# Performance work log

Hardware: AMD Instinct MI355X
Metric: run time of the kernel (lower is better)

## Reference

```python
import jax, jax.numpy as jnp
import numpy as np

BN_EPS = 1e-5

def _tok2img(f):
    # f: [197, 768] tokens (CLS first). Drop CLS, transpose, reshape -> [1, 768, 14, 14].
    # fv4[0, c, i, j] = f[1 + i*14 + j, c], identical to the original triple loop.
    return f[1:].T.reshape(1, 768, 14, 14)

def _resize(x, s):
    # PyTorch F.interpolate(mode='bilinear', align_corners=False) == jax.image.resize 'bilinear'
    n, c, h, w = x.shape
    return jax.image.resize(x, (n, c, h * s, w * s), method='bilinear')

def _conv_relu_bn(x, conv_w, conv_b, g, b, m, v):
    y = jax.lax.conv_general_dilated(x, conv_w, window_strides=(1, 1), padding='SAME',
                                     dimension_numbers=('NCHW', 'OIHW', 'NCHW'))
    y = y + conv_b[None, :, None, None]
    y = jax.nn.relu(y)
    # BatchNorm2d(1) in eval mode with running stats
    scale = g * jax.lax.rsqrt(v + BN_EPS)
    return y * scale[None, :, None, None] + (b - m * scale)[None, :, None, None]

def setup_inputs() -> dict:
    key = jax.random.key(0)
    ks = jax.random.split(key, 4)
    return {
        'x': jax.random.normal(ks[0], (14, 14), dtype=jnp.float32),
        'fv': jax.random.normal(ks[1], (4, 197, 768), dtype=jnp.float32),
        'conv_w': jax.random.normal(ks[2], (1, 769, 3, 3), dtype=jnp.float32) * 0.02,
        'conv_b': jnp.zeros((1,), jnp.float32),
        'bn_gamma': jnp.ones((1,), jnp.float32),
        'bn_beta': jnp.zeros((1,), jnp.float32),
        'bn_mean': jnp.zeros((1,), jnp.float32),
        'bn_var': jnp.ones((1,), jnp.float32),
        'W_w': jax.random.normal(ks[3], (224, 224), dtype=jnp.float32) * 0.05,
        'W_b': jnp.zeros((224,), jnp.float32),
    }

def reference(x, fv, conv_w, conv_b, bn_gamma, bn_beta, bn_mean, bn_var, W_w, W_b):
    h = x[None, None]  # [1,1,14,14]
    # skip features, pre-resized to match current resolution at each stage
    feats = (
        _tok2img(fv[3]),              # 14x14
        _resize(_tok2img(fv[2]), 2),  # 28x28
        _resize(_tok2img(fv[1]), 4),  # 56x56
        _resize(_tok2img(fv[0]), 8),  # 112x112
    )
    for f in feats:
        h = jnp.concatenate([h, f], axis=1)  # [1,769,H,W]
        h = _conv_relu_bn(h, conv_w, conv_b, bn_gamma, bn_beta, bn_mean, bn_var)
        h = _resize(h, 2)
    # Linear(224,224) over the last dim of [1,1,224,224]
    h = jnp.einsum('nchw,ow->ncho', h, W_w) + W_b
    return jax.nn.sigmoid(h)
```

## Files before the change

### kernel.cpp

```cpp
#include <hip/hip_runtime.h>
#include <math.h>


#define BN_EPS 1e-5f

__device__ __forceinline__ float clampf(float x, float lo, float hi) {
    return fminf(fmaxf(x, lo), hi);
}

__device__ __forceinline__ float sampleB(const float* __restrict__ Bt, float fy, float fx) {
    int y0 = (int)fy; float by = fy - (float)y0; int y1 = min(y0 + 1, 13);
    int x0 = (int)fx; float bx = fx - (float)x0; int x1 = min(x0 + 1, 13);
    return (1.f - by) * ((1.f - bx) * Bt[y0 * 14 + x0] + bx * Bt[y0 * 14 + x1])
         + by         * ((1.f - bx) * Bt[y1 * 14 + x0] + bx * Bt[y1 * 14 + x1]);
}

__device__ __forceinline__ float stage_pixel(int i, int j, int H,
                                             const float* __restrict__ hsrc, int srcH, int doUp,
                                             const float* __restrict__ sB,
                                             const float* __restrict__ cw, float bias) {
    float featScale = 14.0f / (float)H;
    float srcMax = (float)(srcH - 1);
    float acc = bias;

#pragma unroll
    for (int a = 0; a < 3; ++a) {
        int p = i + a - 1;
        if (p < 0 || p >= H) continue;
        float fy = clampf(((float)p + 0.5f) * featScale - 0.5f, 0.f, 13.f);
        int hy0 = 0, hy1 = 0; float fhy = 0.f;
        if (doUp) {
            float hy = clampf(((float)p + 0.5f) * 0.5f - 0.5f, 0.f, srcMax);
            hy0 = (int)hy; fhy = hy - (float)hy0; hy1 = min(hy0 + 1, srcH - 1);
        }
#pragma unroll
        for (int bq = 0; bq < 3; ++bq) {
            int q = j + bq - 1;
            if (q < 0 || q >= H) continue;
            int t = a * 3 + bq;

            float fx = clampf(((float)q + 0.5f) * featScale - 0.5f, 0.f, 13.f);
            float bv = sampleB(sB + t * 196, fy, fx);

            float hval;
            if (doUp) {
                float hx = clampf(((float)q + 0.5f) * 0.5f - 0.5f, 0.f, srcMax);
                int hx0 = (int)hx; float fhx = hx - (float)hx0; int hx1 = min(hx0 + 1, srcH - 1);
                hval = (1.f - fhy) * ((1.f - fhx) * hsrc[hy0 * srcH + hx0] + fhx * hsrc[hy0 * srcH + hx1])
                     + fhy         * ((1.f - fhx) * hsrc[hy1 * srcH + hx0] + fhx * hsrc[hy1 * srcH + hx1]);
            } else {
                hval = hsrc[p * srcH + q];
            }
            acc += cw[t] * hval + bv;
        }
    }
    return acc;
}

__device__ __forceinline__ void srcRange(int dlo, int dhi, int srcH, int& slo, int& shi) {
    int H = 2 * srcH;
    int p0 = max(dlo - 1, 0), p1 = min(dhi + 1, H - 1);
    float h0 = fmaxf(((float)p0 + 0.5f) * 0.5f - 0.5f, 0.f);
    float h1 = fmaxf(((float)p1 + 0.5f) * 0.5f - 0.5f, 0.f);
    slo = (int)h0;
    shi = min((int)h1 + 1, srcH - 1);
}

__global__ __launch_bounds__(256)
void compute_B_kernel(const float* __restrict__ fv, const float* __restrict__ conv_w,
                      const float* __restrict__ W_w,
                      float* __restrict__ gB, float* __restrict__ gWT) {
    int blk = blockIdx.x;
    int s = blk / 196;
    int uv = blk % 196;
    const float* fvrow = fv + ((size_t)(3 - s) * 197 + 1 + uv) * 768;
    int tid = threadIdx.x;

    if (tid < 64) {
        int idx = blk * 64 + tid;
        int o = idx / 224, w = idx % 224;
        gWT[w * 224 + o] = W_w[idx];
    }

    float part[9];
#pragma unroll
    for (int t = 0; t < 9; ++t) part[t] = 0.f;
    for (int k = tid; k < 768; k += 256) {
        float fval = fvrow[k];
        const float* w = conv_w + (size_t)(1 + k) * 9;
#pragma unroll
        for (int t = 0; t < 9; ++t) part[t] += fval * w[t];
    }
#pragma unroll
    for (int t = 0; t < 9; ++t) {
#pragma unroll
        for (int off = 32; off > 0; off >>= 1)
            part[t] += __shfl_down(part[t], off, 64);
    }
    __shared__ float red[4][9];
    int wave = tid >> 6, lane = tid & 63;
    if (lane == 0) {
#pragma unroll
        for (int t = 0; t < 9; ++t) red[wave][t] = part[t];
    }
    __syncthreads();
    if (tid < 9)
        gB[s * 1764 + tid * 196 + uv] = red[0][tid] + red[1][tid] + red[2][tid] + red[3][tid];
}

__global__ __launch_bounds__(1024, 1)
void refine_kernel(const float* __restrict__ x,
                   const float* __restrict__ conv_w, const float* __restrict__ conv_b,
                   const float* __restrict__ bng, const float* __restrict__ bnb,
                   const float* __restrict__ bnm, const float* __restrict__ bnv,
                   const float* __restrict__ W_b,
                   const float* __restrict__ gB, const float* __restrict__ gWT,
                   float* __restrict__ out) {
    __shared__ float sB[4 * 9 * 196];
    __shared__ float y1s[196];
    __shared__ float y2s[784];
    __shared__ float y3s[3136];
    __shared__ float y4loc[3 * 112];
    __shared__ float hrow[2][224];
    __shared__ float partial[4][224];

    int tid = threadIdx.x;
    int b = blockIdx.x;

    int y4lo = max(b - 1, 0), y4hi = min(b + 1, 111);
    int r3lo, r3hi; srcRange(y4lo, y4hi, 56, r3lo, r3hi);
    int r2lo, r2hi; srcRange(r3lo, r3hi, 28, r2lo, r2hi);
    int r1lo, r1hi; srcRange(r2lo, r2hi, 14, r1lo, r1hi);

    for (int k = tid; k < 7056; k += 1024) sB[k] = gB[k];

    float cw[9];
#pragma unroll
    for (int t = 0; t < 9; ++t) cw[t] = conv_w[t];
    float bias = conv_b[0];
    float scale = bng[0] * rsqrtf(bnv[0] + BN_EPS);
    float shift = bnb[0] - bnm[0] * scale;
    __syncthreads();

    {
        int n = (r1hi - r1lo + 1) * 14;
        if (tid < n) {
            int i = r1lo + tid / 14, j = tid % 14;
            float acc = stage_pixel(i, j, 14, x, 14, 0, sB, cw, bias);
            y1s[i * 14 + j] = fmaxf(acc, 0.f) * scale + shift;
        }
    }
    __syncthreads();

    {
        int n = (r2hi - r2lo + 1) * 28;
        if (tid < n) {
            int i = r2lo + tid / 28, j = tid % 28;
            float acc = stage_pixel(i, j, 28, y1s, 14, 1, sB + 1764, cw, bias);
            y2s[i * 28 + j] = fmaxf(acc, 0.f) * scale + shift;
        }
    }
    __syncthreads();

    {
        int n = (r3hi - r3lo + 1) * 56;
        if (tid < n) {
            int i = r3lo + tid / 56, j = tid % 56;
            float acc = stage_pixel(i, j, 56, y2s, 28, 1, sB + 2 * 1764, cw, bias);
            y3s[i * 56 + j] = fmaxf(acc, 0.f) * scale + shift;
        }
    }
    __syncthreads();

    {
        int n = (y4hi - y4lo + 1) * 112;
        if (tid < n) {
            int i = y4lo + tid / 112, j = tid % 112;
            float acc = stage_pixel(i, j, 112, y3s, 56, 1, sB + 3 * 1764, cw, bias);
            y4loc[(i - (b - 1)) * 112 + j] = fmaxf(acc, 0.f) * scale + shift;
        }
    }
    __syncthreads();

    if (tid < 2 * 224) {
        int rr = tid / 224, w = tid % 224;
        int r = 2 * b + rr;
        float hy = clampf(((float)r + 0.5f) * 0.5f - 0.5f, 0.f, 111.f);
        int yy0 = (int)hy; float fy = hy - (float)yy0; int yy1 = min(yy0 + 1, 111);
        float hx = clampf(((float)w + 0.5f) * 0.5f - 0.5f, 0.f, 111.f);
        int xx0 = (int)hx; float fx = hx - (float)xx0; int xx1 = min(xx0 + 1, 111);
        int s0 = yy0 - (b - 1), s1 = yy1 - (b - 1);
        hrow[rr][w] = (1.f - fy) * ((1.f - fx) * y4loc[s0 * 112 + xx0] + fx * y4loc[s0 * 112 + xx1])
                    + fy         * ((1.f - fx) * y4loc[s1 * 112 + xx0] + fx * y4loc[s1 * 112 + xx1]);
    }
    __syncthreads();

    if (tid < 896) {
        int q = tid / 224, o = tid % 224;
        int rr = q >> 1, half = q & 1;
        float acc = half ? 0.f : W_b[o];
        const float* hr = hrow[rr];
        int w0 = half * 112;
        for (int w = w0; w < w0 + 112; ++w)
            acc += hr[w] * gWT[w * 224 + o];
        partial[q][o] = acc;
    }
    __syncthreads();

    if (tid < 448) {
        int rr = tid / 224, o = tid % 224;
        float v = partial[rr * 2][o] + partial[rr * 2 + 1][o];
        out[(size_t)(2 * b + rr) * 224 + o] = 1.f / (1.f + expf(-v));
    }
}

extern "C" void kernel_launch(void* const* d_in, const int* in_sizes, int n_in,
                              void* d_out, int out_size, void* d_ws, size_t ws_size,
                              hipStream_t stream) {
    (void)in_sizes; (void)n_in; (void)out_size; (void)ws_size;
    const float* x      = (const float*)d_in[0];
    const float* fv     = (const float*)d_in[1];
    const float* conv_w = (const float*)d_in[2];
    const float* conv_b = (const float*)d_in[3];
    const float* bng    = (const float*)d_in[4];
    const float* bnb    = (const float*)d_in[5];
    const float* bnm    = (const float*)d_in[6];
    const float* bnv    = (const float*)d_in[7];
    const float* W_w    = (const float*)d_in[8];
    const float* W_b    = (const float*)d_in[9];
    float* out = (float*)d_out;

    float* ws  = (float*)d_ws;
    float* gB  = ws;
    float* gWT = ws + 7056;

    compute_B_kernel<<<784, 256, 0, stream>>>(fv, conv_w, W_w, gB, gWT);
    refine_kernel<<<112, 1024, 0, stream>>>(x, conv_w, conv_b, bng, bnb, bnm, bnv,
                                            W_b, gB, gWT, out);
}
```

Before: 90.15 us.

## Fold horizontal upsample into linear weights and load only needed B rows

Precomputes a 112x224 weight matrix that merges the final horizontal bilinear upsample with the Linear layer. The GEMV now runs on the three 112-wide y4 rows, and the vertical interpolation is applied afterwards on the partial results. Each block also copies only the B-table rows its stage ranges need instead of the full 7056-entry table, and stage 1 uses a direct non-interpolated path. The aim is fewer global loads per block and roughly half the GEMV work, at the cost of computing a third y4 row's dot product and extra partial-buffer shared memory.

Measured after the change: 85.89 us. -4.7%, faster.

```diff
diff --git a/kernel.cpp b/kernel.cpp
--- a/kernel.cpp
+++ b/kernel.cpp
@@ -16,7 +16,7 @@
 }
 
 __device__ __forceinline__ float stage_pixel(int i, int j, int H,
-                                             const float* __restrict__ hsrc, int srcH, int doUp,
+                                             const float* __restrict__ hsrc, int srcH,
                                              const float* __restrict__ sB,
                                              const float* __restrict__ cw, float bias) {
     float featScale = 14.0f / (float)H;
@@ -28,11 +28,8 @@
         int p = i + a - 1;
         if (p < 0 || p >= H) continue;
         float fy = clampf(((float)p + 0.5f) * featScale - 0.5f, 0.f, 13.f);
-        int hy0 = 0, hy1 = 0; float fhy = 0.f;
-        if (doUp) {
-            float hy = clampf(((float)p + 0.5f) * 0.5f - 0.5f, 0.f, srcMax);
-            hy0 = (int)hy; fhy = hy - (float)hy0; hy1 = min(hy0 + 1, srcH - 1);
-        }
+        float hy = clampf(((float)p + 0.5f) * 0.5f - 0.5f, 0.f, srcMax);
+        int hy0 = (int)hy; float fhy = hy - (float)hy0; int hy1 = min(hy0 + 1, srcH - 1);
 #pragma unroll
         for (int bq = 0; bq < 3; ++bq) {
             int q = j + bq - 1;
@@ -42,15 +39,10 @@
             float fx = clampf(((float)q + 0.5f) * featScale - 0.5f, 0.f, 13.f);
             float bv = sampleB(sB + t * 196, fy, fx);
 
-            float hval;
-            if (doUp) {
-                float hx = clampf(((float)q + 0.5f) * 0.5f - 0.5f, 0.f, srcMax);
-                int hx0 = (int)hx; float fhx = hx - (float)hx0; int hx1 = min(hx0 + 1, srcH - 1);
-                hval = (1.f - fhy) * ((1.f - fhx) * hsrc[hy0 * srcH + hx0] + fhx * hsrc[hy0 * srcH + hx1])
-                     + fhy         * ((1.f - fhx) * hsrc[hy1 * srcH + hx0] + fhx * hsrc[hy1 * srcH + hx1]);
-            } else {
-                hval = hsrc[p * srcH + q];
-            }
+            float hx = clampf(((float)q + 0.5f) * 0.5f - 0.5f, 0.f, srcMax);
+            int hx0 = (int)hx; float fhx = hx - (float)hx0; int hx1 = min(hx0 + 1, srcH - 1);
+            float hval = (1.f - fhy) * ((1.f - fhx) * hsrc[hy0 * srcH + hx0] + fhx * hsrc[hy0 * srcH + hx1])
+                       + fhy         * ((1.f - fhx) * hsrc[hy1 * srcH + hx0] + fhx * hsrc[hy1 * srcH + hx1]);
             acc += cw[t] * hval + bv;
         }
     }
@@ -66,20 +58,39 @@
     shi = min((int)h1 + 1, srcH - 1);
 }
 
+__device__ __forceinline__ void bRange(int dlo, int dhi, int H, int& lo, int& hi) {
+    float sc = 14.f / (float)H;
+    int p0 = max(dlo - 1, 0), p1 = min(dhi + 1, H - 1);
+    float f0 = clampf(((float)p0 + 0.5f) * sc - 0.5f, 0.f, 13.f);
+    float f1 = clampf(((float)p1 + 0.5f) * sc - 0.5f, 0.f, 13.f);
+    lo = (int)f0;
+    hi = min((int)f1 + 1, 13);
+}
+
 __global__ __launch_bounds__(256)
 void compute_B_kernel(const float* __restrict__ fv, const float* __restrict__ conv_w,
                       const float* __restrict__ W_w,
-                      float* __restrict__ gB, float* __restrict__ gWT) {
+                      float* __restrict__ gB, float* __restrict__ gWTf) {
     int blk = blockIdx.x;
     int s = blk / 196;
     int uv = blk % 196;
     const float* fvrow = fv + ((size_t)(3 - s) * 197 + 1 + uv) * 768;
     int tid = threadIdx.x;
 
-    if (tid < 64) {
-        int idx = blk * 64 + tid;
-        int o = idx / 224, w = idx % 224;
-        gWT[w * 224 + o] = W_w[idx];
+    if (tid < 32) {
+        int idx = blk * 32 + tid;
+        int o = idx % 224, xx = idx / 224;
+        float acc = 0.f;
+#pragma unroll
+        for (int d = -1; d <= 2; ++d) {
+            int w = 2 * xx + d;
+            if (w < 0 || w > 223) continue;
+            float hx = clampf(((float)w + 0.5f) * 0.5f - 0.5f, 0.f, 111.f);
+            int xx0 = (int)hx; float fx = hx - (float)xx0; int xx1 = min(xx0 + 1, 111);
+            float c = (xx0 == xx ? 1.f - fx : 0.f) + (xx1 == xx ? fx : 0.f);
+            acc += c * W_w[o * 224 + w];
+        }
+        gWTf[xx * 224 + o] = acc;
     }
 
     float part[9];
@@ -114,15 +125,14 @@
                    const float* __restrict__ bng, const float* __restrict__ bnb,
                    const float* __restrict__ bnm, const float* __restrict__ bnv,
                    const float* __restrict__ W_b,
-                   const float* __restrict__ gB, const float* __restrict__ gWT,
+                   const float* __restrict__ gB, const float* __restrict__ gWTf,
                    float* __restrict__ out) {
     __shared__ float sB[4 * 9 * 196];
     __shared__ float y1s[196];
     __shared__ float y2s[784];
     __shared__ float y3s[3136];
     __shared__ float y4loc[3 * 112];
-    __shared__ float hrow[2][224];
-    __shared__ float partial[4][224];
+    __shared__ float partial[12 * 224];
 
     int tid = threadIdx.x;
     int b = blockIdx.x;
@@ -132,7 +142,25 @@
     int r2lo, r2hi; srcRange(r3lo, r3hi, 28, r2lo, r2hi);
     int r1lo, r1hi; srcRange(r2lo, r2hi, 14, r1lo, r1hi);
 
-    for (int k = tid; k < 7056; k += 1024) sB[k] = gB[k];
+    int bl0 = max(r1lo - 1, 0), bh0 = min(r1hi + 1, 13);
+    int bl1, bh1; bRange(r2lo, r2hi, 28, bl1, bh1);
+    int bl2, bh2; bRange(r3lo, r3hi, 56, bl2, bh2);
+    int bl3, bh3; bRange(y4lo, y4hi, 112, bl3, bh3);
+
+    {
+        int bl[4] = {bl0, bl1, bl2, bl3}, bh[4] = {bh0, bh1, bh2, bh3};
+#pragma unroll
+        for (int s4 = 0; s4 < 4; ++s4) {
+            int nrw = (bh[s4] - bl[s4] + 1) * 14;
+            int n = 9 * nrw;
+            int base = s4 * 1764 + bl[s4] * 14;
+            for (int e = tid; e < n; e += 1024) {
+                int t = e / nrw, rem = e % nrw;
+                int off = base + t * 196 + rem;
+                sB[off] = gB[off];
+            }
+        }
+    }
 
     float cw[9];
 #pragma unroll
@@ -146,7 +174,19 @@
         int n = (r1hi - r1lo + 1) * 14;
         if (tid < n) {
             int i = r1lo + tid / 14, j = tid % 14;
-            float acc = stage_pixel(i, j, 14, x, 14, 0, sB, cw, bias);
+            float acc = bias;
+#pragma unroll
+            for (int a = 0; a < 3; ++a) {
+                int p = i + a - 1;
+                if (p < 0 || p >= 14) continue;
+#pragma unroll
+                for (int bq = 0; bq < 3; ++bq) {
+                    int q = j + bq - 1;
+                    if (q < 0 || q >= 14) continue;
+                    int t = a * 3 + bq;
+                    acc += cw[t] * x[p * 14 + q] + sB[t * 196 + p * 14 + q];
+                }
+            }
             y1s[i * 14 + j] = fmaxf(acc, 0.f) * scale + shift;
         }
     }
@@ -156,7 +196,7 @@
         int n = (r2hi - r2lo + 1) * 28;
         if (tid < n) {
             int i = r2lo + tid / 28, j = tid % 28;
-            float acc = stage_pixel(i, j, 28, y1s, 14, 1, sB + 1764, cw, bias);
+            float acc = stage_pixel(i, j, 28, y1s, 14, sB + 1764, cw, bias);
             y2s[i * 28 + j] = fmaxf(acc, 0.f) * scale + shift;
         }
     }
@@ -166,7 +206,7 @@
         int n = (r3hi - r3lo + 1) * 56;
         if (tid < n) {
             int i = r3lo + tid / 56, j = tid % 56;
-            float acc = stage_pixel(i, j, 56, y2s, 28, 1, sB + 2 * 1764, cw, bias);
+            float acc = stage_pixel(i, j, 56, y2s, 28, sB + 2 * 1764, cw, bias);
             y3s[i * 56 + j] = fmaxf(acc, 0.f) * scale + shift;
         }
     }
@@ -176,41 +216,40 @@
         int n = (y4hi - y4lo + 1) * 112;
         if (tid < n) {
             int i = y4lo + tid / 112, j = tid % 112;
-            float acc = stage_pixel(i, j, 112, y3s, 56, 1, sB + 3 * 1764, cw, bias);
+            float acc = stage_pixel(i, j, 112, y3s, 56, sB + 3 * 1764, cw, bias);
             y4loc[(i - (b - 1)) * 112 + j] = fmaxf(acc, 0.f) * scale + shift;
         }
     }
     __syncthreads();
 
-    if (tid < 2 * 224) {
-        int rr = tid / 224, w = tid % 224;
+    if (tid < 896) {
+        int kq = tid / 224, o = tid % 224;
+        int k0 = kq * 28;
+        float a0 = 0.f, a1 = 0.f, a2 = 0.f;
+        for (int k = k0; k < k0 + 28; ++k) {
+            float wf = gWTf[k * 224 + o];
+            a0 += y4loc[k] * wf;
+            a1 += y4loc[112 + k] * wf;
+            a2 += y4loc[224 + k] * wf;
+        }
+        partial[(0 * 4 + kq) * 224 + o] = a0;
+        partial[(1 * 4 + kq) * 224 + o] = a1;
+        partial[(2 * 4 + kq) * 224 + o] = a2;
+    }
+    __syncthreads();
+
+    if (tid < 448) {
+        int rr = tid / 224, o = tid % 224;
         int r = 2 * b + rr;
         float hy = clampf(((float)r + 0.5f) * 0.5f - 0.5f, 0.f, 111.f);
         int yy0 = (int)hy; float fy = hy - (float)yy0; int yy1 = min(yy0 + 1, 111);
-        float hx = clampf(((float)w + 0.5f) * 0.5f - 0.5f, 0.f, 111.f);
-        int xx0 = (int)hx; float fx = hx - (float)xx0; int xx1 = min(xx0 + 1, 111);
         int s0 = yy0 - (b - 1), s1 = yy1 - (b - 1);
-        hrow[rr][w] = (1.f - fy) * ((1.f - fx) * y4loc[s0 * 112 + xx0] + fx * y4loc[s0 * 112 + xx1])
-                    + fy         * ((1.f - fx) * y4loc[s1 * 112 + xx0] + fx * y4loc[s1 * 112 + xx1]);
-    }
-    __syncthreads();
-
-    if (tid < 896) {
-        int q = tid / 224, o = tid % 224;
-        int rr = q >> 1, half = q & 1;
-        float acc = half ? 0.f : W_b[o];
-        const float* hr = hrow[rr];
-        int w0 = half * 112;
-        for (int w = w0; w < w0 + 112; ++w)
-            acc += hr[w] * gWT[w * 224 + o];
-        partial[q][o] = acc;
-    }
-    __syncthreads();
-
-    if (tid < 448) {
-        int rr = tid / 224, o = tid % 224;
-        float v = partial[rr * 2][o] + partial[rr * 2 + 1][o];
-        out[(size_t)(2 * b + rr) * 224 + o] = 1.f / (1.f + expf(-v));
+        float D0 = partial[(s0 * 4 + 0) * 224 + o] + partial[(s0 * 4 + 1) * 224 + o]
+                 + partial[(s0 * 4 + 2) * 224 + o] + partial[(s0 * 4 + 3) * 224 + o];
+        float D1 = partial[(s1 * 4 + 0) * 224 + o] + partial[(s1 * 4 + 1) * 224 + o]
+                 + partial[(s1 * 4 + 2) * 224 + o] + partial[(s1 * 4 + 3) * 224 + o];
+        float v = (1.f - fy) * D0 + fy * D1 + W_b[o];
+        out[(size_t)r * 224 + o] = 1.f / (1.f + expf(-v));
     }
 }
 
@@ -230,11 +269,11 @@
     const float* W_b    = (const float*)d_in[9];
     float* out = (float*)d_out;
 
-    float* ws  = (float*)d_ws;
-    float* gB  = ws;
-    float* gWT = ws + 7056;
-
-    compute_B_kernel<<<784, 256, 0, stream>>>(fv, conv_w, W_w, gB, gWT);
+    float* ws   = (float*)d_ws;
+    float* gB   = ws;
+    float* gWTf = ws + 7056;
+
+    compute_B_kernel<<<784, 256, 0, stream>>>(fv, conv_w, W_w, gB, gWTf);
     refine_kernel<<<112, 1024, 0, stream>>>(x, conv_w, conv_b, bng, bnb, bnm, bnv,
-                                            W_b, gB, gWT, out);
-}
+                                            W_b, gB, gWTf, out);
+}
```
